# Kernel optimization log

Hardware: AMD Instinct MI355X
Metric: run time of the kernel (lower is better)

The kernel has to match this reference:

```python
import jax, jax.numpy as jnp
import numpy as np

IN_DIM = 128
LAYER_DIMS = [128, 128]
NUM_SAMPLES = [25, 10]
L0 = 3072
NEG_WEIGHT = 1.0


def setup_inputs() -> dict:
    key = jax.random.key(0)
    ks = jax.random.split(key, 12)
    feat = jax.random.normal(ks[0], (L0, IN_DIM), dtype=jnp.float32)
    nodes = jax.random.randint(ks[1], (L0,), 0, L0)
    nb0 = jnp.arange(L0)
    nb1 = jax.random.randint(ks[2], (L0 * 10,), 0, L0)
    nb2 = jax.random.randint(ks[3], (L0 * 10 * 25,), 0, L0)
    src_idx = jax.random.randint(ks[4], (1024,), 0, L0)
    pos_idx = jax.random.randint(ks[5], (1024,), 0, L0)
    neg_idx = jax.random.randint(ks[6], (512,), 0, L0)
    g = 0.05
    # mean aggregator weights: layer0 in=IN_DIM, layer1 in=2*128 (concat)
    w_self_0 = jax.random.normal(ks[7], (IN_DIM, 128), jnp.float32) * g
    w_neigh_0 = jax.random.normal(ks[8], (IN_DIM, 128), jnp.float32) * g
    w_self_1 = jax.random.normal(ks[9], (256, 128), jnp.float32) * g
    w_neigh_1 = jax.random.normal(ks[10], (256, 128), jnp.float32) * g
    return dict(nodes=nodes, feat=feat, src_idx=src_idx, pos_idx=pos_idx,
                neg_idx=neg_idx, nb0=nb0, nb1=nb1, nb2=nb2,
                w_self_0=w_self_0, w_neigh_0=w_neigh_0,
                w_self_1=w_self_1, w_neigh_1=w_neigh_1)


def _aggregate(hidden, params):
    # GraphSAGE layer stack: at layer l, combine each hop with the mean of its
    # sampled neighbors, concat self/neigh transforms, relu except last layer.
    num_layers = len(NUM_SAMPLES)
    for layer in range(num_layers):
        w_self, w_neigh = params[layer]
        is_last = layer == num_layers - 1
        next_hidden = []
        for hop in range(num_layers - layer):
            s = NUM_SAMPLES[num_layers - hop - 1]
            self_v = hidden[hop]  # [n, d]
            neigh = hidden[hop + 1].reshape(self_v.shape[0], s, self_v.shape[1])
            neigh_mean = jnp.mean(neigh, axis=1)
            h = jnp.concatenate([self_v @ w_self, neigh_mean @ w_neigh], axis=1)
            if not is_last:
                h = jax.nn.relu(h)
            next_hidden.append(h)
        hidden = next_hidden
    return hidden[0]


def _l2_normalize(x, eps=1e-12):
    return x * jax.lax.rsqrt(jnp.maximum(jnp.sum(x * x, axis=1, keepdims=True), eps))


def reference(nodes, feat, src_idx, pos_idx, neg_idx, nb0, nb1, nb2,
              w_self_0, w_neigh_0, w_self_1, w_neigh_1):
    hidden = [feat[nb0], feat[nb1], feat[nb2]]
    params = [(w_self_0, w_neigh_0), (w_self_1, w_neigh_1)]
    output = _aggregate(hidden, params)          # [L0, 256]
    output = _l2_normalize(output)
    src_emb = output[src_idx]                    # [B, 256]
    pos_emb = output[pos_idx]
    neg_emb = output[neg_idx]                    # [Nneg, 256]

    aff = jnp.sum(src_emb * pos_emb, axis=1)     # [B]
    neg_aff = src_emb @ neg_emb.T                # [B, Nneg]

    # MRR via double argsort (tf double top_k equivalent; ties -> positive last)
    aff_all = jnp.concatenate([neg_aff, aff[:, None]], axis=1)
    order = jnp.argsort(-aff_all, axis=1, stable=True)
    ranks = jnp.argsort(order, axis=1, stable=True)
    mrr = jnp.mean(1.0 / (ranks[:, -1].astype(jnp.float32) + 1.0))

    # sigmoid cross-entropy: labels 1 -> softplus(-x); labels 0 -> softplus(x)
    true_xent = jax.nn.softplus(-aff)
    neg_xent = jax.nn.softplus(neg_aff)
    loss = jnp.sum(true_xent) + NEG_WEIGHT * jnp.sum(neg_xent)
    loss = loss / jnp.asarray(src_emb.shape[0], jnp.float32)
    return src_emb, loss, mrr
```

## Files before the change

### kernel.cpp

```cpp
#include <hip/hip_runtime.h>
#include <math.h>

#define L0      3072
#define BATCH   1024
#define NNEG    512


__device__ __forceinline__ float bf2f(unsigned short u) {
  return __uint_as_float(((unsigned)u) << 16);
}
__device__ __forceinline__ void store_out(float v, float* p) { *p = v; }
__device__ __forceinline__ void store_out(float v, unsigned short* p) {
  unsigned x = __float_as_uint(v);
  *p = (unsigned short)((x + 0x7fff + ((x >> 16) & 1)) >> 16);
}

template<int K, int AW, int HOFF, bool NORM, typename OutT>
__global__ __launch_bounds__(512) void k_mm(
    const float* __restrict__ Ain,
    const float* __restrict__ W0, const float* __restrict__ W1,
    OutT* __restrict__ Out, const int ldo, const int outHalfOff,
    float* __restrict__ zbuf, const int zcount) {
  __shared__ float AT[6 * AW];
  __shared__ float rs[8][3];
  const int t = threadIdx.x;
  if (zbuf != nullptr && blockIdx.x == 0)
    for (int z = t; z < zcount; z += 512) zbuf[z] = 0.f;
  const int base = blockIdx.x * 6;
  {
    const float4* __restrict__ src = (const float4*)(Ain + base * AW);
    float4* __restrict__ dst = (float4*)AT;
    for (int idx = t; idx < 6 * AW / 4; idx += 512) dst[idx] = src[idx];
  }
  __syncthreads();

  const int wave = t >> 6;
  const int half = wave >> 2;
  const int colg = (wave >> 1) & 1;
  const int rowg = wave & 1;
  const int rg = rowg * 3;
  const int col = colg * 64 + (t & 63);
  const float* __restrict__ W = (half ? W1 : W0) + col;
  const float* __restrict__ A0 = AT + rg * AW + half * HOFF;

  float acc[3] = {0.f, 0.f, 0.f};
#pragma unroll 4
  for (int d = 0; d < K; d += 4) {
    float4 a[3];
#pragma unroll
    for (int r = 0; r < 3; ++r) a[r] = *(const float4*)&A0[r * AW + d];
    float w[4];
#pragma unroll
    for (int i2 = 0; i2 < 4; ++i2) w[i2] = W[(d + i2) * 128];
#pragma unroll
    for (int i2 = 0; i2 < 4; ++i2)
#pragma unroll
      for (int r = 0; r < 3; ++r)
        acc[r] = fmaf(((const float*)&a[r])[i2], w[i2], acc[r]);
  }

  float scale[3] = {1.f, 1.f, 1.f};
  if (NORM) {
    float p[3];
#pragma unroll
    for (int r = 0; r < 3; ++r) p[r] = acc[r] * acc[r];
#pragma unroll
    for (int off = 32; off > 0; off >>= 1)
#pragma unroll
      for (int r = 0; r < 3; ++r) p[r] += __shfl_xor(p[r], off, 64);
    if ((t & 63) == 0) { rs[wave][0] = p[0]; rs[wave][1] = p[1]; rs[wave][2] = p[2]; }
    __syncthreads();
#pragma unroll
    for (int r = 0; r < 3; ++r) {
      const float s = rs[rowg][r] + rs[rowg + 2][r] + rs[rowg + 4][r] + rs[rowg + 6][r];
      scale[r] = rsqrtf(fmaxf(s, 1e-12f));
    }
  }
  OutT* __restrict__ O = Out + half * outHalfOff;
#pragma unroll
  for (int r = 0; r < 3; ++r)
    store_out(acc[r] * scale[r], &O[(base + rg + r) * ldo + col]);
}

__global__ __launch_bounds__(640) void k_aggregate(
    const unsigned short* __restrict__ X0, const unsigned short* __restrict__ Y0,
    const int* __restrict__ nb0, const int* __restrict__ nb1,
    const int* __restrict__ nb2, float* __restrict__ H) {
  __shared__ float gB[10][128], gC[10][128], gD[10][128];
  const int i = blockIdx.x;
  const int t = threadIdx.x;
  const int n0 = nb0[i];
  const int j = t >> 6;
  const int lam = t & 63;
  const int r = i * 10 + j;
  int myidx = 0;
  if (lam < 25) myidx = nb2[r * 25 + lam];
  else if (lam == 25) myidx = nb1[r];
  const int c8 = lam & 15;
  const int sub = lam >> 4;

  float d8[8];
#pragma unroll
  for (int e = 0; e < 8; ++e) d8[e] = 0.f;
#pragma unroll
  for (int m = 0; m < 7; ++m) {
    const int k = sub + 4 * m;
    const int ridx = __shfl(myidx, k, 64);
    if (k < 25) {
      const float4 raw = *(const float4*)(Y0 + ridx * 128 + c8 * 8);
      const unsigned short* u = (const unsigned short*)&raw;
#pragma unroll
      for (int e = 0; e < 8; ++e) d8[e] += bf2f(u[e]);
    }
  }
#pragma unroll
  for (int e = 0; e < 8; ++e) d8[e] += __shfl_xor(d8[e], 16, 64);
#pragma unroll
  for (int e = 0; e < 8; ++e) d8[e] += __shfl_xor(d8[e], 32, 64);

  const int r1 = __shfl(myidx, 25, 64);
  if (sub == 0) {
#pragma unroll
    for (int e = 0; e < 8; ++e) gD[j][c8 * 8 + e] = fmaxf(d8[e] * 0.04f, 0.f);
    const float4 raw = *(const float4*)(Y0 + r1 * 128 + c8 * 8);
    const unsigned short* u = (const unsigned short*)&raw;
#pragma unroll
    for (int e = 0; e < 8; ++e) gB[j][c8 * 8 + e] = bf2f(u[e]);
  } else if (sub == 1) {
    const float4 raw = *(const float4*)(X0 + r1 * 128 + c8 * 8);
    const unsigned short* u = (const unsigned short*)&raw;
#pragma unroll
    for (int e = 0; e < 8; ++e) gC[j][c8 * 8 + e] = fmaxf(bf2f(u[e]), 0.f);
  }
  __syncthreads();

  if (t < 512) {
    const int q = t >> 7, c = t & 127;
    float v;
    if (q == 0) {
      v = fmaxf(bf2f(X0[n0 * 128 + c]), 0.f);
    } else {
      const float* g = (q == 1) ? &gB[0][0] : (q == 2) ? &gC[0][0] : &gD[0][0];
      float s = 0.f;
#pragma unroll
      for (int jj = 0; jj < 10; ++jj) s += g[jj * 128 + c];
      v = s * 0.1f;
      if (q == 1) v = fmaxf(v, 0.f);
    }
    H[i * 512 + t] = v;
  }
}

__device__ __forceinline__ float softplusf(float x) {
  return fmaxf(x, 0.f) + log1pf(expf(-fabsf(x)));
}

__global__ __launch_bounds__(128) void k_neg(
    const float* __restrict__ O, const int* __restrict__ src_idx,
    const int* __restrict__ pos_idx, const int* __restrict__ neg_idx,
    float* __restrict__ out_src, int* __restrict__ rank,
    float* __restrict__ spPos, float* __restrict__ spNeg,
    int* __restrict__ done) {
  __shared__ float lds[160 * 132];
  __shared__ int rowIdx[160];
  __shared__ float affL[16];
  __shared__ int cntL[16];
  __shared__ float wsum[2];
  __shared__ int lastDone;
  const int t = threadIdx.x;
  const int rowBase = (blockIdx.x >> 2) * 16;
  const int colBase = (blockIdx.x & 3) * 128;
  const bool first = (colBase == 0);

  if (t < 16) { cntL[t] = 0; rowIdx[t] = src_idx[rowBase + t]; }
  else if (t < 32) rowIdx[t] = pos_idx[rowBase + t - 16];
  if (t >= 32) rowIdx[t] = neg_idx[colBase + t - 32];
  if (t < 32) rowIdx[128 + t] = neg_idx[colBase + 96 + t];

  if (first) {
    const float4* __restrict__ s4 = (const float4*)O;
    float4* __restrict__ d4o = (float4*)out_src;
#pragma unroll
    for (int idx = t; idx < 16 * 64; idx += 128) {
      const int rr = idx >> 6, c4 = idx & 63;
      d4o[(rowBase + rr) * 64 + c4] = s4[src_idx[rowBase + rr] * 64 + c4];
    }
  }
  __syncthreads();

  const int tc = t & 31;
  const int tr = t >> 5;
  float acc[4][4];
#pragma unroll
  for (int k = 0; k < 4; ++k)
#pragma unroll
    for (int j = 0; j < 4; ++j) acc[k][j] = 0.f;
  float aff = 0.f;

  for (int ch = 0; ch < 2; ++ch) {
    if (ch) __syncthreads();
    {
      const float4* __restrict__ s4 = (const float4*)O;
#pragma unroll 4
      for (int idx = t; idx < 160 * 32; idx += 128) {
        const int row = idx >> 5, c4 = idx & 31;
        *(float4*)&lds[row * 132 + c4 * 4] = s4[rowIdx[row] * 64 + ch * 32 + c4];
      }
    }
    __syncthreads();
#pragma unroll 2
    for (int d4 = 0; d4 < 32; ++d4) {
      float4 a[4], b[4];
#pragma unroll
      for (int k = 0; k < 4; ++k)
        a[k] = *(const float4*)&lds[(tr + 4 * k) * 132 + d4 * 4];
#pragma unroll
      for (int j = 0; j < 4; ++j)
        b[j] = *(const float4*)&lds[(32 + tc + 32 * j) * 132 + d4 * 4];
      float4 sv, pv;
      if (t < 16) {
        sv = *(const float4*)&lds[t * 132 + d4 * 4];
        pv = *(const float4*)&lds[(16 + t) * 132 + d4 * 4];
      }
#pragma unroll
      for (int i2 = 0; i2 < 4; ++i2) {
#pragma unroll
        for (int k = 0; k < 4; ++k)
#pragma unroll
          for (int j = 0; j < 4; ++j)
            acc[k][j] = fmaf(((const float*)&a[k])[i2],
                             ((const float*)&b[j])[i2], acc[k][j]);
        if (t < 16)
          aff = fmaf(((const float*)&sv)[i2], ((const float*)&pv)[i2], aff);
      }
    }
  }
  if (t < 16) affL[t] = aff;
  __syncthreads();

  float sp = 0.f;
#pragma unroll
  for (int k = 0; k < 4; ++k) {
    const float av = affL[tr + 4 * k];
    int cnt = 0;
#pragma unroll
    for (int j = 0; j < 4; ++j) {
      const float v = acc[k][j];
      sp += softplusf(v);
      cnt += (v >= av) ? 1 : 0;
    }
    if (cnt) atomicAdd(&cntL[tr + 4 * k], cnt);
  }
#pragma unroll
  for (int off = 32; off > 0; off >>= 1) sp += __shfl_down(sp, off, 64);
  if ((t & 63) == 0) wsum[t >> 6] = sp;
  if (first && t < 16) atomicAdd(spPos, softplusf(-aff));
  __syncthreads();
  if (t == 0) atomicAdd(spNeg, wsum[0] + wsum[1]);
  if (t < 16) atomicAdd(&rank[rowBase + t], cntL[t]);

  __threadfence();
  __syncthreads();
  if (t == 0) lastDone = (atomicAdd(done, 1) == 255) ? 1 : 0;
  __syncthreads();
  if (lastDone) {
    float s = 0.f;
    for (int i = t; i < BATCH; i += 128) {
      const int rv = __hip_atomic_load(&rank[i], __ATOMIC_RELAXED,
                                       __HIP_MEMORY_SCOPE_AGENT);
      s += 1.f / (float)(rv + 1);
    }
#pragma unroll
    for (int off = 32; off > 0; off >>= 1) s += __shfl_down(s, off, 64);
    if ((t & 63) == 0) wsum[t >> 6] = s;
    __syncthreads();
    if (t == 0) {
      const float mrr = (wsum[0] + wsum[1]) * (1.f / 1024.f);
      const float p = __hip_atomic_load(spPos, __ATOMIC_RELAXED,
                                        __HIP_MEMORY_SCOPE_AGENT);
      const float n = __hip_atomic_load(spNeg, __ATOMIC_RELAXED,
                                        __HIP_MEMORY_SCOPE_AGENT);
      out_src[BATCH * 256]     = (p + n) * (1.f / 1024.f);
      out_src[BATCH * 256 + 1] = mrr;
    }
  }
}

extern "C" void kernel_launch(void* const* d_in, const int* in_sizes, int n_in,
                              void* d_out, int out_size, void* d_ws, size_t ws_size,
                              hipStream_t stream) {
  const float* feat   = (const float*)d_in[1];
  const int* src_idx  = (const int*)d_in[2];
  const int* pos_idx  = (const int*)d_in[3];
  const int* neg_idx  = (const int*)d_in[4];
  const int* nb0      = (const int*)d_in[5];
  const int* nb1      = (const int*)d_in[6];
  const int* nb2      = (const int*)d_in[7];
  const float* ws0    = (const float*)d_in[8];
  const float* wn0    = (const float*)d_in[9];
  const float* ws1    = (const float*)d_in[10];
  const float* wn1    = (const float*)d_in[11];

  float* wsf = (float*)d_ws;
  unsigned short* X0 = (unsigned short*)d_ws;
  unsigned short* Y0 = X0 + 393216;
  float* H     = wsf + 393216;
  float* R     = wsf + 1966080;
  float* spPos = wsf + 2752512;
  float* spNeg = wsf + 2752513;
  int*   rank  = (int*)(wsf + 2752514);
  int*   done  = rank + 1024;
  float* out   = (float*)d_out;

  k_mm<128, 128, 0, false, unsigned short><<<L0 / 6, 512, 0, stream>>>(
      feat, ws0, wn0, X0, 128, 393216, spPos, 1027);
  k_aggregate<<<L0, 640, 0, stream>>>(X0, Y0, nb0, nb1, nb2, H);
  k_mm<256, 512, 256, true, float><<<L0 / 6, 512, 0, stream>>>(
      H, ws1, wn1, R, 256, 128, nullptr, 0);
  k_neg<<<256, 128, 0, stream>>>(
      R, src_idx, pos_idx, neg_idx, out, rank, spPos, spNeg, done);
}
```

Before: 165.2 us.

## Pre-gather negatives into transposed buffer and stream B from global in k_neg

Adds a k_prep kernel that gathers the 512 negative embeddings and stores them transposed (dim-major) in workspace. k_neg then keeps only the 32 src/pos rows in LDS and reads the negative operand straight from global with coalesced float4 loads. It also doubles the block size to 256 threads with a 2x4 register tile per thread. This cuts the redundant per-block gather of 128 negative rows into LDS and the LDS footprint, which can raise occupancy. The cost is an extra kernel launch and global-memory traffic on the B operand in the inner loop.

After: 166.6 us. Within noise of the previous version (+0.9%).

```diff
diff --git a/kernel.cpp b/kernel.cpp
--- a/kernel.cpp
+++ b/kernel.cpp
@@ -155,33 +155,51 @@
   return fmaxf(x, 0.f) + log1pf(expf(-fabsf(x)));
 }
 
-__global__ __launch_bounds__(128) void k_neg(
-    const float* __restrict__ O, const int* __restrict__ src_idx,
-    const int* __restrict__ pos_idx, const int* __restrict__ neg_idx,
+__global__ __launch_bounds__(256) void k_prep(
+    const float* __restrict__ R, const int* __restrict__ neg_idx,
+    float* __restrict__ NT) {
+  const int idx = blockIdx.x * 256 + threadIdx.x;
+  const int c = idx & 511;
+  const int d4 = idx >> 9;
+  const float4 v = *(const float4*)&R[neg_idx[c] * 256 + d4 * 4];
+#pragma unroll
+  for (int i2 = 0; i2 < 4; ++i2)
+    NT[(d4 * 4 + i2) * 512 + c] = ((const float*)&v)[i2];
+}
+
+__global__ __launch_bounds__(256) void k_neg(
+    const float* __restrict__ O, const float* __restrict__ NT,
+    const int* __restrict__ src_idx, const int* __restrict__ pos_idx,
     float* __restrict__ out_src, int* __restrict__ rank,
     float* __restrict__ spPos, float* __restrict__ spNeg,
     int* __restrict__ done) {
-  __shared__ float lds[160 * 132];
-  __shared__ int rowIdx[160];
+  __shared__ float SP[32 * 260];
   __shared__ float affL[16];
   __shared__ int cntL[16];
-  __shared__ float wsum[2];
+  __shared__ float wsum[4];
   __shared__ int lastDone;
   const int t = threadIdx.x;
   const int rowBase = (blockIdx.x >> 2) * 16;
   const int colBase = (blockIdx.x & 3) * 128;
   const bool first = (colBase == 0);
 
-  if (t < 16) { cntL[t] = 0; rowIdx[t] = src_idx[rowBase + t]; }
-  else if (t < 32) rowIdx[t] = pos_idx[rowBase + t - 16];
-  if (t >= 32) rowIdx[t] = neg_idx[colBase + t - 32];
-  if (t < 32) rowIdx[128 + t] = neg_idx[colBase + 96 + t];
-
+  if (t < 16) cntL[t] = 0;
+
+  {
+    const float4* __restrict__ s4 = (const float4*)O;
+#pragma unroll
+    for (int idx = t; idx < 32 * 64; idx += 256) {
+      const int row = idx >> 6, c4 = idx & 63;
+      const int rid = (row < 16) ? src_idx[rowBase + row]
+                                 : pos_idx[rowBase + row - 16];
+      *(float4*)&SP[row * 260 + c4 * 4] = s4[rid * 64 + c4];
+    }
+  }
   if (first) {
     const float4* __restrict__ s4 = (const float4*)O;
     float4* __restrict__ d4o = (float4*)out_src;
 #pragma unroll
-    for (int idx = t; idx < 16 * 64; idx += 128) {
+    for (int idx = t; idx < 16 * 64; idx += 256) {
       const int rr = idx >> 6, c4 = idx & 63;
       d4o[(rowBase + rr) * 64 + c4] = s4[src_idx[rowBase + rr] * 64 + c4];
     }
@@ -190,73 +208,70 @@
 
   const int tc = t & 31;
   const int tr = t >> 5;
-  float acc[4][4];
-#pragma unroll
-  for (int k = 0; k < 4; ++k)
-#pragma unroll
-    for (int j = 0; j < 4; ++j) acc[k][j] = 0.f;
+  const float* __restrict__ B = NT + colBase + 4 * tc;
+  const float* __restrict__ A0 = SP + tr * 260;
+  const float* __restrict__ A1 = SP + (tr + 8) * 260;
+  const float* __restrict__ SV = SP + t * 260;
+  const float* __restrict__ PV = SP + (16 + t) * 260;
+
+  float acc[2][4];
+#pragma unroll
+  for (int r = 0; r < 2; ++r)
+#pragma unroll
+    for (int j = 0; j < 4; ++j) acc[r][j] = 0.f;
   float aff = 0.f;
 
-  for (int ch = 0; ch < 2; ++ch) {
-    if (ch) __syncthreads();
-    {
-      const float4* __restrict__ s4 = (const float4*)O;
-#pragma unroll 4
-      for (int idx = t; idx < 160 * 32; idx += 128) {
-        const int row = idx >> 5, c4 = idx & 31;
-        *(float4*)&lds[row * 132 + c4 * 4] = s4[rowIdx[row] * 64 + ch * 32 + c4];
+#pragma unroll 2
+  for (int d4 = 0; d4 < 64; ++d4) {
+    const int dd = d4 * 4;
+    const float4 a0 = *(const float4*)&A0[dd];
+    const float4 a1 = *(const float4*)&A1[dd];
+    float4 b[4];
+#pragma unroll
+    for (int i2 = 0; i2 < 4; ++i2)
+      b[i2] = *(const float4*)&B[(dd + i2) * 512];
+    float4 sv, pv;
+    if (t < 16) {
+      sv = *(const float4*)&SV[dd];
+      pv = *(const float4*)&PV[dd];
+    }
+#pragma unroll
+    for (int i2 = 0; i2 < 4; ++i2) {
+      const float va0 = ((const float*)&a0)[i2];
+      const float va1 = ((const float*)&a1)[i2];
+#pragma unroll
+      for (int j = 0; j < 4; ++j) {
+        const float vb = ((const float*)&b[i2])[j];
+        acc[0][j] = fmaf(va0, vb, acc[0][j]);
+        acc[1][j] = fmaf(va1, vb, acc[1][j]);
       }
-    }
-    __syncthreads();
-#pragma unroll 2
-    for (int d4 = 0; d4 < 32; ++d4) {
-      float4 a[4], b[4];
-#pragma unroll
-      for (int k = 0; k < 4; ++k)
-        a[k] = *(const float4*)&lds[(tr + 4 * k) * 132 + d4 * 4];
-#pragma unroll
-      for (int j = 0; j < 4; ++j)
-        b[j] = *(const float4*)&lds[(32 + tc + 32 * j) * 132 + d4 * 4];
-      float4 sv, pv;
-      if (t < 16) {
-        sv = *(const float4*)&lds[t * 132 + d4 * 4];
-        pv = *(const float4*)&lds[(16 + t) * 132 + d4 * 4];
-      }
-#pragma unroll
-      for (int i2 = 0; i2 < 4; ++i2) {
-#pragma unroll
-        for (int k = 0; k < 4; ++k)
-#pragma unroll
-          for (int j = 0; j < 4; ++j)
-            acc[k][j] = fmaf(((const float*)&a[k])[i2],
-                             ((const float*)&b[j])[i2], acc[k][j]);
-        if (t < 16)
-          aff = fmaf(((const float*)&sv)[i2], ((const float*)&pv)[i2], aff);
-      }
+      if (t < 16)
+        aff = fmaf(((const float*)&sv)[i2], ((const float*)&pv)[i2], aff);
     }
   }
   if (t < 16) affL[t] = aff;
   __syncthreads();
 
   float sp = 0.f;
-#pragma unroll
-  for (int k = 0; k < 4; ++k) {
-    const float av = affL[tr + 4 * k];
-    int cnt = 0;
+  int cnt[2] = {0, 0};
+#pragma unroll
+  for (int r = 0; r < 2; ++r) {
+    const float av = affL[tr + 8 * r];
 #pragma unroll
     for (int j = 0; j < 4; ++j) {
-      const float v = acc[k][j];
+      const float v = acc[r][j];
       sp += softplusf(v);
-      cnt += (v >= av) ? 1 : 0;
-    }
-    if (cnt) atomicAdd(&cntL[tr + 4 * k], cnt);
-  }
+      cnt[r] += (v >= av) ? 1 : 0;
+    }
+  }
+  if (cnt[0]) atomicAdd(&cntL[tr], cnt[0]);
+  if (cnt[1]) atomicAdd(&cntL[tr + 8], cnt[1]);
 #pragma unroll
   for (int off = 32; off > 0; off >>= 1) sp += __shfl_down(sp, off, 64);
   if ((t & 63) == 0) wsum[t >> 6] = sp;
   if (first && t < 16) atomicAdd(spPos, softplusf(-aff));
   __syncthreads();
-  if (t == 0) atomicAdd(spNeg, wsum[0] + wsum[1]);
+  if (t == 0) atomicAdd(spNeg, wsum[0] + wsum[1] + wsum[2] + wsum[3]);
   if (t < 16) atomicAdd(&rank[rowBase + t], cntL[t]);
 
   __threadfence();
@@ -265,7 +280,7 @@
   __syncthreads();
   if (lastDone) {
     float s = 0.f;
-    for (int i = t; i < BATCH; i += 128) {
+    for (int i = t; i < BATCH; i += 256) {
       const int rv = __hip_atomic_load(&rank[i], __ATOMIC_RELAXED,
                                        __HIP_MEMORY_SCOPE_AGENT);
       s += 1.f / (float)(rv + 1);
@@ -275,7 +290,7 @@
     if ((t & 63) == 0) wsum[t >> 6] = s;
     __syncthreads();
     if (t == 0) {
-      const float mrr = (wsum[0] + wsum[1]) * (1.f / 1024.f);
+      const float mrr = (wsum[0] + wsum[1] + wsum[2] + wsum[3]) * (1.f / 1024.f);
       const float p = __hip_atomic_load(spPos, __ATOMIC_RELAXED,
                                         __HIP_MEMORY_SCOPE_AGENT);
       const float n = __hip_atomic_load(spNeg, __ATOMIC_RELAXED,
@@ -310,6 +325,7 @@
   float* spNeg = wsf + 2752513;
   int*   rank  = (int*)(wsf + 2752514);
   int*   done  = rank + 1024;
+  float* NT    = wsf + 2753540;
   float* out   = (float*)d_out;
 
   k_mm<128, 128, 0, false, unsigned short><<<L0 / 6, 512, 0, stream>>>(
@@ -317,6 +333,7 @@
   k_aggregate<<<L0, 640, 0, stream>>>(X0, Y0, nb0, nb1, nb2, H);
   k_mm<256, 512, 256, true, float><<<L0 / 6, 512, 0, stream>>>(
       H, ws1, wn1, R, 256, 128, nullptr, 0);
-  k_neg<<<256, 128, 0, stream>>>(
-      R, src_idx, pos_idx, neg_idx, out, rank, spPos, spNeg, done);
-}
+  k_prep<<<128, 256, 0, stream>>>(R, neg_idx, NT);
+  k_neg<<<256, 256, 0, stream>>>(
+      R, NT, src_idx, pos_idx, out, rank, spPos, spNeg, done);
+}
```
